# Performance work log

Measured on AMD Instinct MI355X. Metric: run time of the kernel, lower is better.

Reference implementation:

```python
import jax, jax.numpy as jnp
import numpy as np

B, T, D, H = 4, 4096, 1024, 16
HD = D // H  # head_dim = 64


def setup_inputs() -> dict:
    key = jax.random.key(0)
    k1, k2, k3 = jax.random.split(key, 3)
    x = jax.random.normal(k1, (B, T, D), dtype=jnp.float32)
    # torch Linear weight is (out,in); we store transposed (in,out) for x @ W
    Wqkv = jax.random.normal(k2, (D, 3 * D), dtype=jnp.float32) * 0.02
    Wout = jax.random.normal(k3, (D, D), dtype=jnp.float32) * 0.02
    return {"x": x, "Wqkv": Wqkv, "Wout": Wout}


def reference(x, Wqkv, Wout):
    # Faithful to original: qkv reshaped to (B,T,3,H,hd) WITHOUT moving heads to
    # a batch dim, so attention mixes the H heads of each token (scores: B,T,H,H).
    qkv = (x @ Wqkv).reshape(B, T, 3, H, HD)
    q, k, v = qkv[:, :, 0], qkv[:, :, 1], qkv[:, :, 2]  # each (B,T,H,HD)
    scores = jnp.einsum('btid,btjd->btij', q, k) / jnp.sqrt(jnp.float32(HD))
    attn = jax.nn.softmax(scores, axis=-1)  # softmax over heads j
    out = jnp.einsum('btij,btjd->btid', attn, v).reshape(B, T, D)
    return out @ Wout
```

## Files before the change

kernel.cpp:

```cpp
#include <hip/hip_runtime.h>
#include <hip/hip_bf16.h>
#include <cstdint>
#include <cstddef>


typedef __bf16 bf16x8 __attribute__((ext_vector_type(8)));
typedef __bf16 bf16x4 __attribute__((ext_vector_type(4)));
typedef float  f32x4  __attribute__((ext_vector_type(4)));

#define AS1 __attribute__((address_space(1)))
#define AS3 __attribute__((address_space(3)))

__device__ __forceinline__ void async_copy16(const void* g, void* l) {
    __builtin_amdgcn_global_load_lds((const AS1 void*)g, (AS3 void*)l, 16, 0, 0);
}

__device__ __forceinline__ int invp_qkv(int col) {
    int g = col >> 10;
    if (g == 2) { int q = col & 1023; return 2048 + ((q & 63) << 4) + (q >> 6); }
    int h = (col >> 6) & 15, d = col & 63;
    return (g << 10) + ((d & 32) << 4) + (((d >> 3) & 3) << 7) + (h << 3) + (d & 7);
}

__device__ __forceinline__ int invp_ao(int k) {
    return (((k >> 8) & 3) << 8) + ((k & 15) << 4) + (((k >> 4) & 3) << 2) + ((k >> 6) & 3);
}

__global__ __launch_bounds__(256) void cvt_bf16_kernel(const float4* __restrict__ in,
                                                       bf16x4* __restrict__ out, int n4) {
    int i = blockIdx.x * 256 + threadIdx.x;
    if (i >= n4) return;
    float4 v = in[i];
    bf16x4 o = { (__bf16)v.x, (__bf16)v.y, (__bf16)v.z, (__bf16)v.w };
    out[i] = o;
}

__global__ __launch_bounds__(256) void transpose_qkv_kernel(const float* __restrict__ in,
                                                            __bf16* __restrict__ out) {
    __shared__ float tile[32][33];
    const int C = 3072;
    int c0 = blockIdx.x * 32, r0 = blockIdx.y * 32;
    int tx = threadIdx.x, ty = threadIdx.y;
    #pragma unroll
    for (int i = 0; i < 32; i += 8)
        tile[ty + i][tx] = in[(size_t)(r0 + ty + i) * C + c0 + tx];
    __syncthreads();
    #pragma unroll
    for (int i = 0; i < 32; i += 8) {
        int prow = invp_qkv(c0 + ty + i);
        out[(size_t)prow * 1024 + r0 + tx] = (__bf16)tile[tx][ty + i];
    }
}

__global__ __launch_bounds__(256) void transpose_wout_kernel(const float* __restrict__ in,
                                                             __bf16* __restrict__ out) {
    __shared__ float tile[32][33];
    const int C = 1024;
    int c0 = blockIdx.x * 32, r0 = blockIdx.y * 32;
    int tx = threadIdx.x, ty = threadIdx.y;
    #pragma unroll
    for (int i = 0; i < 32; i += 8)
        tile[ty + i][tx] = in[(size_t)(r0 + ty + i) * C + c0 + tx];
    __syncthreads();
    int pk = invp_ao(r0 + tx);
    #pragma unroll
    for (int i = 0; i < 32; i += 8)
        out[(size_t)(c0 + ty + i) * 1024 + pk] = (__bf16)tile[tx][ty + i];
}

template<int OUT_BF16>
__global__ __launch_bounds__(256) void gemm_bt(const __bf16* __restrict__ A,
                                               const __bf16* __restrict__ Bt,
                                               void* __restrict__ Cv,
                                               int N, int K) {
    __shared__ __bf16 As[128 * 64];
    __shared__ __bf16 Bs[128 * 64];

    const int lin = blockIdx.x;
    const int xcd = lin & 7;
    const int rr  = lin >> 3;
    const int by  = xcd * 16 + (rr & 15);
    const int bx  = rr >> 4;

    const int tid  = threadIdx.x;
    const int wave = tid >> 6;
    const int lane = tid & 63;
    const int quad = lane >> 4;
    const int q16  = lane & 15;
    const int wr   = wave >> 1, wc = wave & 1;
    const int row0 = by * 128;
    const int col0 = bx * 128;

    const __bf16* Ag = A  + (size_t)row0 * K;
    const __bf16* Bg = Bt + (size_t)col0 * K;

    const int l8 = lane >> 3;
    const int l7 = lane & 7;
    const int srow = wave * 8 + l8;
    const int skoff = (l7 ^ l8) << 3;
    char* dstA = (char*)As + wave * 1024;
    char* dstB = (char*)Bs + wave * 1024;

    const int rx = q16 & 7;

    f32x4 acc[4][4] = {};

    for (int k0 = 0; k0 < K; k0 += 64) {
        #pragma unroll
        for (int g = 0; g < 4; ++g) {
            const size_t roff = (size_t)(g * 32 + srow) * K + (k0 + skoff);
            async_copy16(Ag + roff, dstA + g * 4096);
            async_copy16(Bg + roff, dstB + g * 4096);
        }
        __syncthreads();

        #pragma unroll
        for (int s = 0; s < 2; ++s) {
            const int ps = (s * 4 + quad);
            bf16x8 af[4], bfr[4];
            #pragma unroll
            for (int mi = 0; mi < 4; ++mi) {
                int row = wr * 64 + mi * 16 + q16;
                af[mi] = *(const bf16x8*)((const char*)As + row * 128 + ((ps ^ rx) << 4));
            }
            #pragma unroll
            for (int ni = 0; ni < 4; ++ni) {
                int row = wc * 64 + ni * 16 + q16;
                bfr[ni] = *(const bf16x8*)((const char*)Bs + row * 128 + ((ps ^ rx) << 4));
            }
            #pragma unroll
            for (int mi = 0; mi < 4; ++mi)
                #pragma unroll
                for (int ni = 0; ni < 4; ++ni)
                    acc[mi][ni] = __builtin_amdgcn_mfma_f32_16x16x32_bf16(af[mi], bfr[ni], acc[mi][ni], 0, 0, 0);
        }
        __syncthreads();
    }

    #pragma unroll
    for (int mi = 0; mi < 4; ++mi) {
        #pragma unroll
        for (int ni = 0; ni < 4; ++ni) {
            int col = col0 + wc * 64 + ni * 16 + q16;
            #pragma unroll
            for (int r = 0; r < 4; ++r) {
                int row = row0 + wr * 64 + mi * 16 + quad * 4 + r;
                if (OUT_BF16)
                    ((__bf16*)Cv)[(size_t)row * N + col] = (__bf16)acc[mi][ni][r];
                else
                    ((float*)Cv)[(size_t)row * N + col] = acc[mi][ni][r];
            }
        }
    }
}

__global__ __launch_bounds__(256) void attn_mfma_kernel(const __bf16* __restrict__ qkv,
                                                        __bf16* __restrict__ ao) {
    const int tok  = blockIdx.x * 4 + (threadIdx.x >> 6);
    const int lane = threadIdx.x & 63;
    const int quad = lane >> 4;
    const int q16  = lane & 15;

    const __bf16* base = qkv + (size_t)tok * 3072;

    const bf16x8 qf0 = *(const bf16x8*)(base + lane * 8);
    const bf16x8 qf1 = *(const bf16x8*)(base + 512 + lane * 8);
    const bf16x8 kf0 = *(const bf16x8*)(base + 1024 + lane * 8);
    const bf16x8 kf1 = *(const bf16x8*)(base + 1536 + lane * 8);

    f32x4 st = {0.f, 0.f, 0.f, 0.f};
    st = __builtin_amdgcn_mfma_f32_16x16x32_bf16(kf0, qf0, st, 0, 0, 0);
    st = __builtin_amdgcn_mfma_f32_16x16x32_bf16(kf1, qf1, st, 0, 0, 0);

    float s0 = st[0] * 0.125f, s1 = st[1] * 0.125f, s2 = st[2] * 0.125f, s3 = st[3] * 0.125f;
    float m = fmaxf(fmaxf(s0, s1), fmaxf(s2, s3));
    m = fmaxf(m, __shfl_xor(m, 16));
    m = fmaxf(m, __shfl_xor(m, 32));
    float e0 = __expf(s0 - m), e1 = __expf(s1 - m), e2 = __expf(s2 - m), e3 = __expf(s3 - m);
    float sum = e0 + e1 + e2 + e3;
    sum += __shfl_xor(sum, 16);
    sum += __shfl_xor(sum, 32);
    const float inv = 1.f / sum;

    union { __bf16 h[2]; int i; } u01, u23;
    u01.h[0] = (__bf16)(e0 * inv); u01.h[1] = (__bf16)(e1 * inv);
    u23.h[0] = (__bf16)(e2 * inv); u23.h[1] = (__bf16)(e3 * inv);

    const int src0 = quad * 32 + q16;
    const int src1 = src0 + 16;
    union { int i[4]; bf16x8 v; } af;
    af.i[0] = __shfl(u01.i, src0);
    af.i[1] = __shfl(u23.i, src0);
    af.i[2] = __shfl(u01.i, src1);
    af.i[3] = __shfl(u23.i, src1);
    if (quad >= 2) { af.i[0] = 0; af.i[1] = 0; af.i[2] = 0; af.i[3] = 0; }

    const __bf16* vb = base + 2048;
    f32x4 accs[4];
    #pragma unroll
    for (int c = 0; c < 4; ++c) {
        bf16x8 bfv = {};
        if (quad < 2)
            bfv = *(const bf16x8*)(vb + (c * 16 + q16) * 16 + quad * 8);
        f32x4 z = {0.f, 0.f, 0.f, 0.f};
        accs[c] = __builtin_amdgcn_mfma_f32_16x16x32_bf16(af.v, bfv, z, 0, 0, 0);
    }

    union { __bf16 h[16]; bf16x8 v[2]; } o;
    #pragma unroll
    for (int c = 0; c < 4; ++c)
        #pragma unroll
        for (int r = 0; r < 4; ++r)
            o.h[c * 4 + r] = (__bf16)accs[c][r];
    __bf16* outp = ao + (size_t)tok * 1024 + lane * 16;
    *(bf16x8*)outp = o.v[0];
    *(bf16x8*)(outp + 8) = o.v[1];
}

extern "C" void kernel_launch(void* const* d_in, const int* in_sizes, int n_in,
                              void* d_out, int out_size, void* d_ws, size_t ws_size,
                              hipStream_t stream) {
    const float* x    = (const float*)d_in[0];
    const float* Wqkv = (const float*)d_in[1];
    const float* Wout = (const float*)d_in[2];
    float* out = (float*)d_out;

    char* ws = (char*)d_ws;
    __bf16* xb    = (__bf16*)(ws);
    __bf16* wqkvT = (__bf16*)(ws + 33554432);
    __bf16* woutT = (__bf16*)(ws + 33554432 + 6291456);
    __bf16* qkv   = (__bf16*)(ws + 33554432 + 6291456 + 2097152);
    __bf16* ao    = (__bf16*)(ws + 33554432 + 6291456 + 2097152 + 100663296);

    cvt_bf16_kernel<<<16384, 256, 0, stream>>>((const float4*)x, (bf16x4*)xb, 4194304);
    transpose_qkv_kernel<<<dim3(96, 32), dim3(32, 8), 0, stream>>>(Wqkv, wqkvT);
    transpose_wout_kernel<<<dim3(32, 32), dim3(32, 8), 0, stream>>>(Wout, woutT);
    gemm_bt<1><<<24 * 128, 256, 0, stream>>>(xb, wqkvT, (void*)qkv, 3072, 1024);
    attn_mfma_kernel<<<4096, 256, 0, stream>>>(qkv, ao);
    gemm_bt<0><<<8 * 128, 256, 0, stream>>>(ao, woutT, (void*)out, 1024, 1024);
}
```

Measured before the change: 318.2 us.

## Add producer wave with double-buffered LDS and flag sync to GEMM

Replaces the synchronous load-then-compute GEMM loop with a warp-specialized design. A fifth wave issues async global-to-LDS copies into a double buffer, while four compute waves spin on LDS flags and signal buffer release with atomics. The aim is to overlap the next tile's memory loads with the current tile's MFMA work and drop the block-wide barriers. In exchange it doubles LDS use, which may lower occupancy, adds spin-wait overhead, and depends on hand-coded waitcnt immediates being correct.

```diff
diff --git a/kernel.cpp b/kernel.cpp
--- a/kernel.cpp
+++ b/kernel.cpp
@@ -21,7 +21,6 @@
     int h = (col >> 6) & 15, d = col & 63;
     return (g << 10) + ((d & 32) << 4) + (((d >> 3) & 3) << 7) + (h << 3) + (d & 7);
 }
-
 __device__ __forceinline__ int invp_ao(int k) {
     return (((k >> 8) & 3) << 8) + ((k & 15) << 4) + (((k >> 4) & 3) << 2) + ((k >> 6) & 3);
 }
@@ -69,12 +68,13 @@
 }
 
 template<int OUT_BF16>
-__global__ __launch_bounds__(256) void gemm_bt(const __bf16* __restrict__ A,
+__global__ __launch_bounds__(320) void gemm_pc(const __bf16* __restrict__ A,
                                                const __bf16* __restrict__ Bt,
                                                void* __restrict__ Cv,
                                                int N, int K) {
-    __shared__ __bf16 As[128 * 64];
-    __shared__ __bf16 Bs[128 * 64];
+    __shared__ __bf16 As[2][128 * 64];
+    __shared__ __bf16 Bs[2][128 * 64];
+    __shared__ int flags[8];
 
     const int lin = blockIdx.x;
     const int xcd = lin & 7;
@@ -85,70 +85,100 @@
     const int tid  = threadIdx.x;
     const int wave = tid >> 6;
     const int lane = tid & 63;
-    const int quad = lane >> 4;
-    const int q16  = lane & 15;
-    const int wr   = wave >> 1, wc = wave & 1;
-    const int row0 = by * 128;
-    const int col0 = bx * 128;
-
-    const __bf16* Ag = A  + (size_t)row0 * K;
-    const __bf16* Bg = Bt + (size_t)col0 * K;
-
-    const int l8 = lane >> 3;
-    const int l7 = lane & 7;
-    const int srow = wave * 8 + l8;
-    const int skoff = (l7 ^ l8) << 3;
-    char* dstA = (char*)As + wave * 1024;
-    char* dstB = (char*)Bs + wave * 1024;
-
-    const int rx = q16 & 7;
-
-    f32x4 acc[4][4] = {};
-
-    for (int k0 = 0; k0 < K; k0 += 64) {
+
+    if (tid == 0) { flags[0] = flags[1] = flags[4] = flags[5] = 0; }
+    __syncthreads();
+
+    const int T = K >> 6;
+
+    if (wave == 4) {
+        const int l8 = lane >> 3, l7 = lane & 7;
+        const int koff = (l7 ^ l8) << 3;
+        const __bf16* Ag = A  + (size_t)(by * 128 + l8) * K + koff;
+        const __bf16* Bg = Bt + (size_t)(bx * 128 + l8) * K + koff;
+
+        auto issue = [&](int t) {
+            const int b = t & 1;
+            const size_t kk = (size_t)t * 64;
+            char* da = (char*)As[b];
+            char* db = (char*)Bs[b];
+            #pragma unroll
+            for (int i = 0; i < 16; ++i)
+                async_copy16(Ag + (size_t)i * 8 * K + kk, da + i * 1024);
+            #pragma unroll
+            for (int i = 0; i < 16; ++i)
+                async_copy16(Bg + (size_t)i * 8 * K + kk, db + i * 1024);
+        };
+
+        issue(0);
+        for (int t = 0; t < T; ++t) {
+            if (t + 1 < T) {
+                const int b1 = (t + 1) & 1;
+                const int need = 4 * ((t + 1) >> 1);
+                while (__hip_atomic_load(&flags[4 + b1], __ATOMIC_ACQUIRE,
+                                         __HIP_MEMORY_SCOPE_WORKGROUP) < need) {}
+                issue(t + 1);
+                __builtin_amdgcn_s_waitcnt(0x8F70);
+            } else {
+                __builtin_amdgcn_s_waitcnt(0x0F70);
+            }
+            if (lane == 0)
+                __hip_atomic_store(&flags[t & 1], t + 1, __ATOMIC_RELEASE,
+                                   __HIP_MEMORY_SCOPE_WORKGROUP);
+        }
+    } else {
+        const int quad = lane >> 4;
+        const int q16  = lane & 15;
+        const int wr   = wave >> 1, wc = wave & 1;
+        const int rx   = q16 & 7;
+
+        f32x4 acc[4][4] = {};
+
+        for (int t = 0; t < T; ++t) {
+            const int b = t & 1;
+            while (__hip_atomic_load(&flags[b], __ATOMIC_ACQUIRE,
+                                     __HIP_MEMORY_SCOPE_WORKGROUP) < t + 1) {}
+            const char* Ab = (const char*)As[b];
+            const char* Bb = (const char*)Bs[b];
+            #pragma unroll
+            for (int s = 0; s < 2; ++s) {
+                const int ps = s * 4 + quad;
+                bf16x8 af[4], bfr[4];
+                #pragma unroll
+                for (int mi = 0; mi < 4; ++mi) {
+                    int row = wr * 64 + mi * 16 + q16;
+                    af[mi] = *(const bf16x8*)(Ab + row * 128 + ((ps ^ rx) << 4));
+                }
+                #pragma unroll
+                for (int ni = 0; ni < 4; ++ni) {
+                    int row = wc * 64 + ni * 16 + q16;
+                    bfr[ni] = *(const bf16x8*)(Bb + row * 128 + ((ps ^ rx) << 4));
+                }
+                #pragma unroll
+                for (int mi = 0; mi < 4; ++mi)
+                    #pragma unroll
+                    for (int ni = 0; ni < 4; ++ni)
+                        acc[mi][ni] = __builtin_amdgcn_mfma_f32_16x16x32_bf16(af[mi], bfr[ni], acc[mi][ni], 0, 0, 0);
+            }
+            if (lane == 0)
+                __hip_atomic_fetch_add(&flags[4 + b], 1, __ATOMIC_ACQ_REL,
+                                       __HIP_MEMORY_SCOPE_WORKGROUP);
+        }
+
+        const int row0 = by * 128, col0 = bx * 128;
         #pragma unroll
-        for (int g = 0; g < 4; ++g) {
-            const size_t roff = (size_t)(g * 32 + srow) * K + (k0 + skoff);
-            async_copy16(Ag + roff, dstA + g * 4096);
-            async_copy16(Bg + roff, dstB + g * 4096);
-        }
-        __syncthreads();
-
-        #pragma unroll
-        for (int s = 0; s < 2; ++s) {
-            const int ps = (s * 4 + quad);
-            bf16x8 af[4], bfr[4];
-            #pragma unroll
-            for (int mi = 0; mi < 4; ++mi) {
-                int row = wr * 64 + mi * 16 + q16;
-                af[mi] = *(const bf16x8*)((const char*)As + row * 128 + ((ps ^ rx) << 4));
-            }
+        for (int mi = 0; mi < 4; ++mi) {
             #pragma unroll
             for (int ni = 0; ni < 4; ++ni) {
-                int row = wc * 64 + ni * 16 + q16;
-                bfr[ni] = *(const bf16x8*)((const char*)Bs + row * 128 + ((ps ^ rx) << 4));
-            }
-            #pragma unroll
-            for (int mi = 0; mi < 4; ++mi)
-                #pragma unroll
-                for (int ni = 0; ni < 4; ++ni)
-                    acc[mi][ni] = __builtin_amdgcn_mfma_f32_16x16x32_bf16(af[mi], bfr[ni], acc[mi][ni], 0, 0, 0);
-        }
-        __syncthreads();
-    }
-
-    #pragma unroll
-    for (int mi = 0; mi < 4; ++mi) {
-        #pragma unroll
-        for (int ni = 0; ni < 4; ++ni) {
-            int col = col0 + wc * 64 + ni * 16 + q16;
-            #pragma unroll
-            for (int r = 0; r < 4; ++r) {
-                int row = row0 + wr * 64 + mi * 16 + quad * 4 + r;
-                if (OUT_BF16)
-                    ((__bf16*)Cv)[(size_t)row * N + col] = (__bf16)acc[mi][ni][r];
-                else
-                    ((float*)Cv)[(size_t)row * N + col] = acc[mi][ni][r];
+                int col = col0 + wc * 64 + ni * 16 + q16;
+                #pragma unroll
+                for (int r = 0; r < 4; ++r) {
+                    int row = row0 + wr * 64 + mi * 16 + quad * 4 + r;
+                    if (OUT_BF16)
+                        ((__bf16*)Cv)[(size_t)row * N + col] = (__bf16)acc[mi][ni][r];
+                    else
+                        ((float*)Cv)[(size_t)row * N + col] = acc[mi][ni][r];
+                }
             }
         }
     }
@@ -235,7 +265,7 @@
     cvt_bf16_kernel<<<16384, 256, 0, stream>>>((const float4*)x, (bf16x4*)xb, 4194304);
     transpose_qkv_kernel<<<dim3(96, 32), dim3(32, 8), 0, stream>>>(Wqkv, wqkvT);
     transpose_wout_kernel<<<dim3(32, 32), dim3(32, 8), 0, stream>>>(Wout, woutT);
-    gemm_bt<1><<<24 * 128, 256, 0, stream>>>(xb, wqkvT, (void*)qkv, 3072, 1024);
+    gemm_pc<1><<<24 * 128, 320, 0, stream>>>(xb, wqkvT, (void*)qkv, 3072, 1024);
     attn_mfma_kernel<<<4096, 256, 0, stream>>>(qkv, ao);
-    gemm_bt<0><<<8 * 128, 256, 0, stream>>>(ao, woutT, (void*)out, 1024, 1024);
-}
+    gemm_pc<0><<<8 * 128, 320, 0, stream>>>(ao, woutT, (void*)out, 1024, 1024);
+}
```

After: 459.4 us. +44.4%, slower.
